# Kernel tuning notes

Measured on AMD Instinct MI355X. Metric: run time of the kernel, lower is better.

## Reference

```python
import jax, jax.numpy as jnp
import numpy as np

ALPHA = 0.2  # LeakyReLU negative slope


def setup_inputs() -> dict:
    key = jax.random.key(0)
    k1, k2, k3, k4, k5 = jax.random.split(key, 5)
    E, R, F = 256, 16, 64
    return {
        "h": jax.random.normal(k1, (E, F), dtype=jnp.float32),
        "r": jax.random.normal(k2, (R, F), dtype=jnp.float32),
        "adj": jax.random.normal(k3, (E, E, R), dtype=jnp.float32),
        "w_lin": jax.random.normal(k4, (1, F), dtype=jnp.float32) * (1.0 / np.sqrt(F)),
        "b_lin": jax.random.normal(k5, (1,), dtype=jnp.float32),
    }


def reference(h, r, adj, w_lin, b_lin):
    E, F = h.shape
    R = r.shape[0]
    # a_input[i,j,k,f] = h[i,f] * r[k,f] * h[j,f]   (torch repeat/view algebra)
    a_input = h[:, None, None, :] * h[None, :, None, :] * r[None, None, :, :]  # (E,E,R,F)
    adj_agg = jax.nn.softmax(adj, axis=1)  # (E,E,R)
    # leakyrelu over the big tensor, then reduce over the first E axis -> (E,R,F)
    attention = jnp.sum(jax.nn.leaky_relu(adj_agg[..., None] * a_input, ALPHA), axis=0)
    attention_E = jax.nn.softmax(attention, axis=0)  # softmax over E
    attention_R = jax.nn.softmax(attention, axis=1)  # softmax over R
    # linear (F -> 1) then torch .view(R, E, -1): a reshape, NOT a transpose
    alpha = (attention_R @ w_lin.T + b_lin).reshape(R, E, 1)
    alpha = jax.nn.softmax(alpha, axis=1)
    h_prime = jnp.sum(attention_E * h[:, None, :], axis=1)  # (E,F)
    r_prime = jnp.sum(attention_R * r[None, :, :], axis=0)  # (R,F)
    return jax.nn.elu(h_prime), jax.nn.elu(r_prime), alpha
```

## Files before the change

kernel.cpp:

```cpp
#include <hip/hip_runtime.h>
#include <math.h>

#define E 256
#define R 16
#define F 64

__device__ __forceinline__ float eluf(float x) {
  return x > 0.f ? x : expm1f(x);
}

__global__ __launch_bounds__(256) void k1_adj_softmax(const float* __restrict__ adj,
                                                      float* __restrict__ s) {
  __shared__ float lds[256 * 17];
  __shared__ float red[256];
  __shared__ float mk[16], sk[16];
  const int i = blockIdx.x;
  const int t = threadIdx.x;
  const float* a = adj + i * 4096;
  for (int q = 0; q < 16; ++q) {
    int l = q * 256 + t;
    lds[(l >> 4) * 17 + (l & 15)] = a[l];
  }
  __syncthreads();
  const int k = t & 15, g = t >> 4;
  float m = -INFINITY;
  #pragma unroll
  for (int jj = 0; jj < 16; ++jj) m = fmaxf(m, lds[(g * 16 + jj) * 17 + k]);
  red[k * 16 + g] = m;
  __syncthreads();
  if (t < 16) {
    float mm = red[t * 16];
    for (int g2 = 1; g2 < 16; ++g2) mm = fmaxf(mm, red[t * 16 + g2]);
    mk[t] = mm;
  }
  __syncthreads();
  const float mm = mk[k];
  float ssum = 0.f;
  #pragma unroll
  for (int jj = 0; jj < 16; ++jj) {
    int idx = (g * 16 + jj) * 17 + k;
    float v = __expf(lds[idx] - mm);
    lds[idx] = v;
    ssum += v;
  }
  red[k * 16 + g] = ssum;
  __syncthreads();
  if (t < 16) {
    float ss = 0.f;
    for (int g2 = 0; g2 < 16; ++g2) ss += red[t * 16 + g2];
    sk[t] = 1.f / ss;
  }
  __syncthreads();
  float* so = s + i * 4096;
  for (int q = 0; q < 16; ++q) {
    int l = q * 256 + t;
    int kk = l & 15;
    so[l] = lds[(l >> 4) * 17 + kk] * sk[kk];
  }
}

__global__ __launch_bounds__(256) void k2_contract(const float* __restrict__ h,
                                                   const float* __restrict__ r,
                                                   const float* __restrict__ s,
                                                   float* __restrict__ att) {
  __shared__ float hl[E * F];
  __shared__ float sl[E * R];
  __shared__ float redp[4 * 16 * 4 * 17];
  __shared__ float redq[4 * 16 * 4 * 17];
  const int j = blockIdx.x;
  const int t = threadIdx.x;

  float4* hl4 = (float4*)hl;
  const float4* h4 = (const float4*)h;
  #pragma unroll
  for (int q = 0; q < 16; ++q) hl4[q * 256 + t] = h4[q * 256 + t];
  float4* sl4 = (float4*)sl;
  const float4* s4 = (const float4*)s;
  #pragma unroll
  for (int q = 0; q < 4; ++q) {
    int c = q * 256 + t;
    sl4[c] = s4[(c >> 2) * 1024 + j * 4 + (c & 3)];
  }
  __syncthreads();

  const int kg = t >> 6;
  const int ig = (t >> 4) & 3;
  const int fg = t & 15;
  float p[4][4] = {{0.f}};
  float qa[4][4] = {{0.f}};
  const int ibase = ig * 64;
  for (int ii = 0; ii < 64; ++ii) {
    const int i = ibase + ii;
    const float4 hv = *(const float4*)&hl[i * F + fg * 4];
    const float4 sv = *(const float4*)&sl[i * R + kg * 4];
    const float hvv[4] = {hv.x, hv.y, hv.z, hv.w};
    const float hav[4] = {fabsf(hv.x), fabsf(hv.y), fabsf(hv.z), fabsf(hv.w)};
    const float svv[4] = {sv.x, sv.y, sv.z, sv.w};
    #pragma unroll
    for (int kk = 0; kk < 4; ++kk) {
      #pragma unroll
      for (int ff = 0; ff < 4; ++ff) {
        p[kk][ff]  = fmaf(svv[kk], hvv[ff], p[kk][ff]);
        qa[kk][ff] = fmaf(svv[kk], hav[ff], qa[kk][ff]);
      }
    }
  }
  {
    float* rp = &redp[((kg * 16 + fg) * 4 + ig) * 17];
    float* rq = &redq[((kg * 16 + fg) * 4 + ig) * 17];
    #pragma unroll
    for (int kk = 0; kk < 4; ++kk)
      #pragma unroll
      for (int ff = 0; ff < 4; ++ff) {
        rp[kk * 4 + ff] = p[kk][ff];
        rq[kk * 4 + ff] = qa[kk][ff];
      }
  }
  __syncthreads();
  #pragma unroll
  for (int qq = 0; qq < 4; ++qq) {
    const int kf = qq * 256 + t;
    const int k = kf >> 6, f = kf & 63;
    const int base = ((k >> 2) * 16 + (f >> 2)) * 4 * 17 + (k & 3) * 4 + (f & 3);
    float pv = redp[base] + redp[base + 17] + redp[base + 34] + redp[base + 51];
    float qv = redq[base] + redq[base + 17] + redq[base + 34] + redq[base + 51];
    const float c = hl[j * F + f] * r[k * F + f];
    att[j * 1024 + kf] = 0.6f * c * pv + 0.4f * fabsf(c) * qv;
  }
}

__global__ __launch_bounds__(256) void k3_rowsoft(const float* __restrict__ att,
                                                  const float* __restrict__ w,
                                                  const float* __restrict__ b,
                                                  float* __restrict__ aR,
                                                  float* __restrict__ lin) {
  const int e = blockIdx.x;
  const int t = threadIdx.x;
  const int f = t & 63;
  const int wv = t >> 6;
  const float* ar = att + e * 1024;
  float av[16];
  #pragma unroll
  for (int k = 0; k < 16; ++k) av[k] = ar[k * 64 + f];
  float m = -INFINITY;
  #pragma unroll
  for (int k = 0; k < 16; ++k) m = fmaxf(m, av[k]);
  float ssum = 0.f;
  float ex[16];
  #pragma unroll
  for (int k = 0; k < 16; ++k) { ex[k] = __expf(av[k] - m); ssum += ex[k]; }
  const float inv = 1.f / ssum;
  const float wf = w[f];
  const float bb = b[0];
  #pragma unroll
  for (int mq = 0; mq < 4; ++mq) {
    const int k = wv * 4 + mq;
    const float a = ex[k] * inv;
    aR[e * 1024 + k * 64 + f] = a;
    float v = a * wf;
    #pragma unroll
    for (int off = 32; off; off >>= 1) v += __shfl_xor(v, off, 64);
    if (f == 0) lin[e * 16 + k] = v + bb;
  }
}

__global__ __launch_bounds__(64) void k4_stats(const float* __restrict__ att,
                                               const float* __restrict__ aR,
                                               const float* __restrict__ lin,
                                               const float* __restrict__ r,
                                               float* __restrict__ M,
                                               float* __restrict__ Sinv,
                                               float* __restrict__ out) {
  const int bid = blockIdx.x;
  const int l = threadIdx.x;
  if (bid < 1024) {
    const int kf = bid;
    float v[4];
    #pragma unroll
    for (int q = 0; q < 4; ++q) v[q] = att[(l + q * 64) * 1024 + kf];
    float m = fmaxf(fmaxf(v[0], v[1]), fmaxf(v[2], v[3]));
    #pragma unroll
    for (int off = 32; off; off >>= 1) m = fmaxf(m, __shfl_xor(m, off, 64));
    float ssum = 0.f;
    #pragma unroll
    for (int q = 0; q < 4; ++q) ssum += __expf(v[q] - m);
    #pragma unroll
    for (int off = 32; off; off >>= 1) ssum += __shfl_xor(ssum, off, 64);
    float rs = 0.f;
    #pragma unroll
    for (int q = 0; q < 4; ++q) rs += aR[(l + q * 64) * 1024 + kf];
    #pragma unroll
    for (int off = 32; off; off >>= 1) rs += __shfl_xor(rs, off, 64);
    if (l == 0) {
      M[kf] = m;
      Sinv[kf] = 1.f / ssum;
      out[16384 + kf] = eluf(r[kf] * rs);
    }
  } else {
    const int a = bid - 1024;
    const float* lrow = lin + a * 256;
    float v[4];
    #pragma unroll
    for (int q = 0; q < 4; ++q) v[q] = lrow[l + q * 64];
    float m = fmaxf(fmaxf(v[0], v[1]), fmaxf(v[2], v[3]));
    #pragma unroll
    for (int off = 32; off; off >>= 1) m = fmaxf(m, __shfl_xor(m, off, 64));
    float ssum = 0.f;
    float ex[4];
    #pragma unroll
    for (int q = 0; q < 4; ++q) { ex[q] = __expf(v[q] - m); ssum += ex[q]; }
    #pragma unroll
    for (int off = 32; off; off >>= 1) ssum += __shfl_xor(ssum, off, 64);
    const float inv = 1.f / ssum;
    #pragma unroll
    for (int q = 0; q < 4; ++q) out[17408 + a * 256 + l + q * 64] = ex[q] * inv;
  }
}

__global__ __launch_bounds__(256) void k5_hprime(const float* __restrict__ att,
                                                 const float* __restrict__ h,
                                                 const float* __restrict__ M,
                                                 const float* __restrict__ Sinv,
                                                 float* __restrict__ out) {
  const int n = blockIdx.x * 256 + threadIdx.x;
  const int e = n >> 6, f = n & 63;
  float ssum = 0.f;
  #pragma unroll
  for (int k = 0; k < 16; ++k) {
    const int kf = k * 64 + f;
    ssum += __expf(att[e * 1024 + kf] - M[kf]) * Sinv[kf];
  }
  out[n] = eluf(h[n] * ssum);
}

extern "C" void kernel_launch(void* const* d_in, const int* in_sizes, int n_in,
                              void* d_out, int out_size, void* d_ws, size_t ws_size,
                              hipStream_t stream) {
  (void)in_sizes; (void)n_in; (void)out_size; (void)ws_size;
  const float* h   = (const float*)d_in[0];
  const float* r   = (const float*)d_in[1];
  const float* adj = (const float*)d_in[2];
  const float* w   = (const float*)d_in[3];
  const float* b   = (const float*)d_in[4];
  float* out = (float*)d_out;

  float* ws   = (float*)d_ws;
  float* s    = ws;
  float* aR   = ws;
  float* att  = ws + 1048576;
  float* lin  = ws + 1310720;
  float* M    = ws + 1314816;
  float* Sinv = ws + 1315840;

  hipLaunchKernelGGL(k1_adj_softmax, dim3(256),  dim3(256), 0, stream, adj, s);
  hipLaunchKernelGGL(k2_contract,    dim3(256),  dim3(256), 0, stream, h, r, s, att);
  hipLaunchKernelGGL(k3_rowsoft,     dim3(256),  dim3(256), 0, stream, att, w, b, aR, lin);
  hipLaunchKernelGGL(k4_stats,       dim3(1040), dim3(64),  0, stream, att, aR, lin, r, M, Sinv, out);
  hipLaunchKernelGGL(k5_hprime,      dim3(64),   dim3(256), 0, stream, att, h, M, Sinv, out);
}
```

Baseline: 87.47 us.

## Fuse five kernels into one cooperative kernel with grid-wide syncs

Replaces the five separate launches with a single cooperative kernel of 256 blocks that uses grid.sync between phases. The row softmax and linear projection are fused into the contraction phase, reusing the att tile held in LDS. The adj softmax is rewritten to reduce with register shuffles, the contraction's cross-group reduction now uses shuffles instead of LDS, and the stats phase is remapped to 256 blocks. This removes launch gaps and one global round trip of att, at the cost of grid barrier overhead and the occupancy limit that cooperative launch imposes.

Result: slower. 183.8 us (+110.1%).

```diff
diff --git a/kernel.cpp b/kernel.cpp
--- a/kernel.cpp
+++ b/kernel.cpp
@@ -1,236 +1,235 @@
 #include <hip/hip_runtime.h>
+#include <hip/hip_cooperative_groups.h>
 #include <math.h>
 
-#define E 256
-#define R 16
-#define F 64
-
-__device__ __forceinline__ float eluf(float x) {
-  return x > 0.f ? x : expm1f(x);
-}
-
-__global__ __launch_bounds__(256) void k1_adj_softmax(const float* __restrict__ adj,
-                                                      float* __restrict__ s) {
-  __shared__ float lds[256 * 17];
+namespace cg = cooperative_groups;
+
+
+__device__ __forceinline__ float eluf(float x) { return x > 0.f ? x : expm1f(x); }
+
+__global__ __launch_bounds__(256) void mega(
+    const float* __restrict__ h, const float* __restrict__ r,
+    const float* __restrict__ adj, const float* __restrict__ w,
+    const float* __restrict__ bias, float* __restrict__ out,
+    float* __restrict__ s, float* __restrict__ att, float* __restrict__ aR,
+    float* __restrict__ lin, float* __restrict__ M, float* __restrict__ Sinv) {
+  cg::grid_group grid = cg::this_grid();
+  __shared__ float hl[256 * 64];
+  __shared__ float sl[256 * 16];
+  __shared__ float rl[16 * 64];
+  __shared__ float attl[16 * 68];
   __shared__ float red[256];
-  __shared__ float mk[16], sk[16];
-  const int i = blockIdx.x;
+
+  const int b = blockIdx.x;
   const int t = threadIdx.x;
-  const float* a = adj + i * 4096;
-  for (int q = 0; q < 16; ++q) {
-    int l = q * 256 + t;
-    lds[(l >> 4) * 17 + (l & 15)] = a[l];
-  }
-  __syncthreads();
-  const int k = t & 15, g = t >> 4;
-  float m = -INFINITY;
-  #pragma unroll
-  for (int jj = 0; jj < 16; ++jj) m = fmaxf(m, lds[(g * 16 + jj) * 17 + k]);
-  red[k * 16 + g] = m;
-  __syncthreads();
-  if (t < 16) {
-    float mm = red[t * 16];
-    for (int g2 = 1; g2 < 16; ++g2) mm = fmaxf(mm, red[t * 16 + g2]);
-    mk[t] = mm;
-  }
-  __syncthreads();
-  const float mm = mk[k];
-  float ssum = 0.f;
-  #pragma unroll
-  for (int jj = 0; jj < 16; ++jj) {
-    int idx = (g * 16 + jj) * 17 + k;
-    float v = __expf(lds[idx] - mm);
-    lds[idx] = v;
-    ssum += v;
-  }
-  red[k * 16 + g] = ssum;
-  __syncthreads();
-  if (t < 16) {
-    float ss = 0.f;
-    for (int g2 = 0; g2 < 16; ++g2) ss += red[t * 16 + g2];
-    sk[t] = 1.f / ss;
-  }
-  __syncthreads();
-  float* so = s + i * 4096;
-  for (int q = 0; q < 16; ++q) {
-    int l = q * 256 + t;
-    int kk = l & 15;
-    so[l] = lds[(l >> 4) * 17 + kk] * sk[kk];
-  }
-}
-
-__global__ __launch_bounds__(256) void k2_contract(const float* __restrict__ h,
-                                                   const float* __restrict__ r,
-                                                   const float* __restrict__ s,
-                                                   float* __restrict__ att) {
-  __shared__ float hl[E * F];
-  __shared__ float sl[E * R];
-  __shared__ float redp[4 * 16 * 4 * 17];
-  __shared__ float redq[4 * 16 * 4 * 17];
-  const int j = blockIdx.x;
-  const int t = threadIdx.x;
-
-  float4* hl4 = (float4*)hl;
-  const float4* h4 = (const float4*)h;
-  #pragma unroll
-  for (int q = 0; q < 16; ++q) hl4[q * 256 + t] = h4[q * 256 + t];
-  float4* sl4 = (float4*)sl;
-  const float4* s4 = (const float4*)s;
-  #pragma unroll
-  for (int q = 0; q < 4; ++q) {
-    int c = q * 256 + t;
-    sl4[c] = s4[(c >> 2) * 1024 + j * 4 + (c & 3)];
-  }
-  __syncthreads();
-
-  const int kg = t >> 6;
-  const int ig = (t >> 4) & 3;
-  const int fg = t & 15;
-  float p[4][4] = {{0.f}};
-  float qa[4][4] = {{0.f}};
-  const int ibase = ig * 64;
-  for (int ii = 0; ii < 64; ++ii) {
-    const int i = ibase + ii;
-    const float4 hv = *(const float4*)&hl[i * F + fg * 4];
-    const float4 sv = *(const float4*)&sl[i * R + kg * 4];
-    const float hvv[4] = {hv.x, hv.y, hv.z, hv.w};
-    const float hav[4] = {fabsf(hv.x), fabsf(hv.y), fabsf(hv.z), fabsf(hv.w)};
-    const float svv[4] = {sv.x, sv.y, sv.z, sv.w};
-    #pragma unroll
-    for (int kk = 0; kk < 4; ++kk) {
-      #pragma unroll
-      for (int ff = 0; ff < 4; ++ff) {
-        p[kk][ff]  = fmaf(svv[kk], hvv[ff], p[kk][ff]);
-        qa[kk][ff] = fmaf(svv[kk], hav[ff], qa[kk][ff]);
+  const int lane = t & 63;
+  const int wv = t >> 6;
+
+  {
+    float v[16];
+    const float4* a4 = (const float4*)(adj + b * 4096 + t * 16);
+    float4 x0 = a4[0], x1 = a4[1], x2 = a4[2], x3 = a4[3];
+    v[0]=x0.x; v[1]=x0.y; v[2]=x0.z; v[3]=x0.w;
+    v[4]=x1.x; v[5]=x1.y; v[6]=x1.z; v[7]=x1.w;
+    v[8]=x2.x; v[9]=x2.y; v[10]=x2.z; v[11]=x2.w;
+    v[12]=x3.x; v[13]=x3.y; v[14]=x3.z; v[15]=x3.w;
+    float m[16];
+    #pragma unroll
+    for (int k=0;k<16;++k) m[k]=v[k];
+    #pragma unroll
+    for (int off=1; off<64; off<<=1)
+      #pragma unroll
+      for (int k=0;k<16;++k) m[k] = fmaxf(m[k], __shfl_xor(m[k], off, 64));
+    if (lane == 0) {
+      #pragma unroll
+      for (int k=0;k<16;++k) red[wv*16+k] = m[k];
+    }
+    __syncthreads();
+    float sum[16];
+    #pragma unroll
+    for (int k=0;k<16;++k) {
+      const float mk = fmaxf(fmaxf(red[k], red[16+k]), fmaxf(red[32+k], red[48+k]));
+      v[k] = __expf(v[k] - mk);
+      sum[k] = v[k];
+    }
+    #pragma unroll
+    for (int off=1; off<64; off<<=1)
+      #pragma unroll
+      for (int k=0;k<16;++k) sum[k] += __shfl_xor(sum[k], off, 64);
+    __syncthreads();
+    if (lane == 0) {
+      #pragma unroll
+      for (int k=0;k<16;++k) red[wv*16+k] = sum[k];
+    }
+    __syncthreads();
+    #pragma unroll
+    for (int k=0;k<16;++k) {
+      const float sk = red[k]+red[16+k]+red[32+k]+red[48+k];
+      v[k] *= (1.f / sk);
+    }
+    float4* so4 = (float4*)(s + b*4096 + t*16);
+    so4[0] = make_float4(v[0],v[1],v[2],v[3]);
+    so4[1] = make_float4(v[4],v[5],v[6],v[7]);
+    so4[2] = make_float4(v[8],v[9],v[10],v[11]);
+    so4[3] = make_float4(v[12],v[13],v[14],v[15]);
+  }
+  grid.sync();
+
+  {
+    const int j = b;
+    float4* hl4 = (float4*)hl;
+    const float4* h4 = (const float4*)h;
+    #pragma unroll
+    for (int q=0;q<16;++q) hl4[q*256+t] = h4[q*256+t];
+    ((float4*)rl)[t] = ((const float4*)r)[t];
+    float4* sl4 = (float4*)sl;
+    const float4* s4c = (const float4*)s;
+    #pragma unroll
+    for (int q=0;q<4;++q) {
+      const int c = q*256+t;
+      sl4[c] = s4c[(c>>2)*1024 + j*4 + (c&3)];
+    }
+    __syncthreads();
+    const int kg = t>>6, ig=(t>>4)&3, fg=t&15;
+    float p[4][4] = {};
+    float qa[4][4] = {};
+    const int ibase = ig*64;
+    #pragma unroll 8
+    for (int ii=0; ii<64; ++ii) {
+      const int i = ibase + ii;
+      const float4 hv = *(const float4*)&hl[i*64 + fg*4];
+      const float4 sv = *(const float4*)&sl[i*16 + kg*4];
+      const float hvv[4] = {hv.x,hv.y,hv.z,hv.w};
+      const float hav[4] = {fabsf(hv.x),fabsf(hv.y),fabsf(hv.z),fabsf(hv.w)};
+      const float svv[4] = {sv.x,sv.y,sv.z,sv.w};
+      #pragma unroll
+      for (int kk=0;kk<4;++kk)
+        #pragma unroll
+        for (int ff=0;ff<4;++ff) {
+          p[kk][ff]  = fmaf(svv[kk], hvv[ff], p[kk][ff]);
+          qa[kk][ff] = fmaf(svv[kk], hav[ff], qa[kk][ff]);
+        }
+    }
+    #pragma unroll
+    for (int kk=0;kk<4;++kk)
+      #pragma unroll
+      for (int ff=0;ff<4;++ff) {
+        float pv = p[kk][ff];
+        pv += __shfl_xor(pv, 16, 64);
+        pv += __shfl_xor(pv, 32, 64);
+        float qv = qa[kk][ff];
+        qv += __shfl_xor(qv, 16, 64);
+        qv += __shfl_xor(qv, 32, 64);
+        if (ig == 0) {
+          const int k = kg*4+kk, f = fg*4+ff;
+          const float c = hl[j*64+f] * rl[k*64+f];
+          attl[k*68+f] = 0.6f*c*pv + 0.4f*fabsf(c)*qv;
+        }
       }
-    }
-  }
-  {
-    float* rp = &redp[((kg * 16 + fg) * 4 + ig) * 17];
-    float* rq = &redq[((kg * 16 + fg) * 4 + ig) * 17];
-    #pragma unroll
-    for (int kk = 0; kk < 4; ++kk)
-      #pragma unroll
-      for (int ff = 0; ff < 4; ++ff) {
-        rp[kk * 4 + ff] = p[kk][ff];
-        rq[kk * 4 + ff] = qa[kk][ff];
-      }
-  }
-  __syncthreads();
-  #pragma unroll
-  for (int qq = 0; qq < 4; ++qq) {
-    const int kf = qq * 256 + t;
-    const int k = kf >> 6, f = kf & 63;
-    const int base = ((k >> 2) * 16 + (f >> 2)) * 4 * 17 + (k & 3) * 4 + (f & 3);
-    float pv = redp[base] + redp[base + 17] + redp[base + 34] + redp[base + 51];
-    float qv = redq[base] + redq[base + 17] + redq[base + 34] + redq[base + 51];
-    const float c = hl[j * F + f] * r[k * F + f];
-    att[j * 1024 + kf] = 0.6f * c * pv + 0.4f * fabsf(c) * qv;
-  }
-}
-
-__global__ __launch_bounds__(256) void k3_rowsoft(const float* __restrict__ att,
-                                                  const float* __restrict__ w,
-                                                  const float* __restrict__ b,
-                                                  float* __restrict__ aR,
-                                                  float* __restrict__ lin) {
-  const int e = blockIdx.x;
-  const int t = threadIdx.x;
-  const int f = t & 63;
-  const int wv = t >> 6;
-  const float* ar = att + e * 1024;
-  float av[16];
-  #pragma unroll
-  for (int k = 0; k < 16; ++k) av[k] = ar[k * 64 + f];
-  float m = -INFINITY;
-  #pragma unroll
-  for (int k = 0; k < 16; ++k) m = fmaxf(m, av[k]);
-  float ssum = 0.f;
-  float ex[16];
-  #pragma unroll
-  for (int k = 0; k < 16; ++k) { ex[k] = __expf(av[k] - m); ssum += ex[k]; }
-  const float inv = 1.f / ssum;
-  const float wf = w[f];
-  const float bb = b[0];
-  #pragma unroll
-  for (int mq = 0; mq < 4; ++mq) {
-    const int k = wv * 4 + mq;
-    const float a = ex[k] * inv;
-    aR[e * 1024 + k * 64 + f] = a;
-    float v = a * wf;
-    #pragma unroll
-    for (int off = 32; off; off >>= 1) v += __shfl_xor(v, off, 64);
-    if (f == 0) lin[e * 16 + k] = v + bb;
-  }
-}
-
-__global__ __launch_bounds__(64) void k4_stats(const float* __restrict__ att,
-                                               const float* __restrict__ aR,
-                                               const float* __restrict__ lin,
-                                               const float* __restrict__ r,
-                                               float* __restrict__ M,
-                                               float* __restrict__ Sinv,
-                                               float* __restrict__ out) {
-  const int bid = blockIdx.x;
-  const int l = threadIdx.x;
-  if (bid < 1024) {
-    const int kf = bid;
-    float v[4];
-    #pragma unroll
-    for (int q = 0; q < 4; ++q) v[q] = att[(l + q * 64) * 1024 + kf];
-    float m = fmaxf(fmaxf(v[0], v[1]), fmaxf(v[2], v[3]));
-    #pragma unroll
-    for (int off = 32; off; off >>= 1) m = fmaxf(m, __shfl_xor(m, off, 64));
+    __syncthreads();
+    #pragma unroll
+    for (int q=0;q<4;++q) {
+      const int kf = q*256 + t;
+      att[j*1024 + kf] = attl[(kf>>6)*68 + (kf&63)];
+    }
+    float av[16];
+    #pragma unroll
+    for (int k=0;k<16;++k) av[k] = attl[k*68 + lane];
+    float mr = av[0];
+    #pragma unroll
+    for (int k=1;k<16;++k) mr = fmaxf(mr, av[k]);
     float ssum = 0.f;
     #pragma unroll
-    for (int q = 0; q < 4; ++q) ssum += __expf(v[q] - m);
-    #pragma unroll
-    for (int off = 32; off; off >>= 1) ssum += __shfl_xor(ssum, off, 64);
-    float rs = 0.f;
-    #pragma unroll
-    for (int q = 0; q < 4; ++q) rs += aR[(l + q * 64) * 1024 + kf];
-    #pragma unroll
-    for (int off = 32; off; off >>= 1) rs += __shfl_xor(rs, off, 64);
-    if (l == 0) {
-      M[kf] = m;
-      Sinv[kf] = 1.f / ssum;
-      out[16384 + kf] = eluf(r[kf] * rs);
-    }
-  } else {
-    const int a = bid - 1024;
-    const float* lrow = lin + a * 256;
-    float v[4];
-    #pragma unroll
-    for (int q = 0; q < 4; ++q) v[q] = lrow[l + q * 64];
-    float m = fmaxf(fmaxf(v[0], v[1]), fmaxf(v[2], v[3]));
-    #pragma unroll
-    for (int off = 32; off; off >>= 1) m = fmaxf(m, __shfl_xor(m, off, 64));
+    for (int k=0;k<16;++k) ssum += __expf(av[k]-mr);
+    const float inv = 1.f/ssum;
+    const float wf = w[lane];
+    const float bb = bias[0];
+    #pragma unroll
+    for (int mq=0; mq<4; ++mq) {
+      const int k = wv*4 + mq;
+      const float a = __expf(attl[k*68 + lane] - mr) * inv;
+      aR[j*1024 + k*64 + lane] = a;
+      float vsum = a * wf;
+      #pragma unroll
+      for (int off=1; off<64; off<<=1) vsum += __shfl_xor(vsum, off, 64);
+      if (lane == 0) lin[j*16 + k] = vsum + bb;
+    }
+  }
+  grid.sync();
+
+  {
+    const int c = t & 3;
+    const int kf = b*4 + c;
+    const int er = t >> 2;
+    float av[4], rv[4];
+    #pragma unroll
+    for (int q=0;q<4;++q) {
+      const int e = er + (q<<6);
+      av[q] = att[e*1024 + kf];
+      rv[q] = aR[e*1024 + kf];
+    }
+    float m = fmaxf(fmaxf(av[0],av[1]), fmaxf(av[2],av[3]));
+    #pragma unroll
+    for (int off=4; off<64; off<<=1) m = fmaxf(m, __shfl_xor(m, off, 64));
+    if (lane < 4) red[wv*4 + c] = m;
+    __syncthreads();
+    const float mc = fmaxf(fmaxf(red[c], red[4+c]), fmaxf(red[8+c], red[12+c]));
+    float es = __expf(av[0]-mc)+__expf(av[1]-mc)+__expf(av[2]-mc)+__expf(av[3]-mc);
+    float rs = rv[0]+rv[1]+rv[2]+rv[3];
+    #pragma unroll
+    for (int off=4; off<64; off<<=1) {
+      es += __shfl_xor(es, off, 64);
+      rs += __shfl_xor(rs, off, 64);
+    }
+    __syncthreads();
+    if (lane < 4) { red[wv*8 + c] = es; red[wv*8 + 4 + c] = rs; }
+    __syncthreads();
+    if (t < 4) {
+      const int kf2 = b*4 + t;
+      const float S  = red[t] + red[8+t] + red[16+t] + red[24+t];
+      const float RS = red[4+t] + red[12+t] + red[20+t] + red[28+t];
+      M[kf2] = mc;
+      Sinv[kf2] = 1.f/S;
+      out[16384 + kf2] = eluf(r[kf2]*RS);
+    }
+  }
+  if (b < 16) {
+    __syncthreads();
+    const float lv = lin[b*256 + t];
+    float m2 = lv;
+    #pragma unroll
+    for (int off=1; off<64; off<<=1) m2 = fmaxf(m2, __shfl_xor(m2, off, 64));
+    if (lane == 0) red[wv] = m2;
+    __syncthreads();
+    m2 = fmaxf(fmaxf(red[0],red[1]), fmaxf(red[2],red[3]));
+    const float ex = __expf(lv - m2);
+    float ss = ex;
+    #pragma unroll
+    for (int off=1; off<64; off<<=1) ss += __shfl_xor(ss, off, 64);
+    __syncthreads();
+    if (lane == 0) red[wv] = ss;
+    __syncthreads();
+    ss = red[0]+red[1]+red[2]+red[3];
+    out[17408 + b*256 + t] = ex * (1.f/ss);
+  }
+  grid.sync();
+
+  {
+    const int e = b;
+    const int f = lane;
     float ssum = 0.f;
-    float ex[4];
-    #pragma unroll
-    for (int q = 0; q < 4; ++q) { ex[q] = __expf(v[q] - m); ssum += ex[q]; }
-    #pragma unroll
-    for (int off = 32; off; off >>= 1) ssum += __shfl_xor(ssum, off, 64);
-    const float inv = 1.f / ssum;
-    #pragma unroll
-    for (int q = 0; q < 4; ++q) out[17408 + a * 256 + l + q * 64] = ex[q] * inv;
-  }
-}
-
-__global__ __launch_bounds__(256) void k5_hprime(const float* __restrict__ att,
-                                                 const float* __restrict__ h,
-                                                 const float* __restrict__ M,
-                                                 const float* __restrict__ Sinv,
-                                                 float* __restrict__ out) {
-  const int n = blockIdx.x * 256 + threadIdx.x;
-  const int e = n >> 6, f = n & 63;
-  float ssum = 0.f;
-  #pragma unroll
-  for (int k = 0; k < 16; ++k) {
-    const int kf = k * 64 + f;
-    ssum += __expf(att[e * 1024 + kf] - M[kf]) * Sinv[kf];
-  }
-  out[n] = eluf(h[n] * ssum);
+    #pragma unroll
+    for (int kk=0;kk<4;++kk) {
+      const int kf = (wv*4+kk)*64 + f;
+      ssum += __expf(att[e*1024 + kf] - M[kf]) * Sinv[kf];
+    }
+    red[wv*64 + f] = ssum;
+    __syncthreads();
+    if (wv == 0) {
+      const float tot = red[f] + red[64+f] + red[128+f] + red[192+f];
+      out[e*64 + f] = eluf(h[e*64 + f] * tot);
+    }
+  }
 }
 
 extern "C" void kernel_launch(void* const* d_in, const int* in_sizes, int n_in,
@@ -241,20 +240,19 @@
   const float* r   = (const float*)d_in[1];
   const float* adj = (const float*)d_in[2];
   const float* w   = (const float*)d_in[3];
-  const float* b   = (const float*)d_in[4];
+  const float* bi  = (const float*)d_in[4];
   float* out = (float*)d_out;
 
   float* ws   = (float*)d_ws;
   float* s    = ws;
-  float* aR   = ws;
   float* att  = ws + 1048576;
-  float* lin  = ws + 1310720;
-  float* M    = ws + 1314816;
-  float* Sinv = ws + 1315840;
-
-  hipLaunchKernelGGL(k1_adj_softmax, dim3(256),  dim3(256), 0, stream, adj, s);
-  hipLaunchKernelGGL(k2_contract,    dim3(256),  dim3(256), 0, stream, h, r, s, att);
-  hipLaunchKernelGGL(k3_rowsoft,     dim3(256),  dim3(256), 0, stream, att, w, b, aR, lin);
-  hipLaunchKernelGGL(k4_stats,       dim3(1040), dim3(64),  0, stream, att, aR, lin, r, M, Sinv, out);
-  hipLaunchKernelGGL(k5_hprime,      dim3(64),   dim3(256), 0, stream, att, h, M, Sinv, out);
+  float* aR   = ws + 1310720;
+  float* lin  = ws + 1572864;
+  float* M    = ws + 1576960;
+  float* Sinv = ws + 1577984;
+
+  void* args[] = {(void*)&h, (void*)&r, (void*)&adj, (void*)&w, (void*)&bi,
+                  (void*)&out, (void*)&s, (void*)&att, (void*)&aR, (void*)&lin,
+                  (void*)&M, (void*)&Sinv};
+  hipLaunchCooperativeKernel((const void*)mega, dim3(256), dim3(256), args, 0, stream);
 }
```
